# Performance work log

Hardware: AMD Instinct MI355X
Metric: run time of the kernel (lower is better)

## Reference

```python
import jax, jax.numpy as jnp
import numpy as np

NEG_INF = -1e30  # underflows to exactly 0 after softmax in fp32, matching -inf masking


def setup_inputs() -> dict:
    key = jax.random.key(0)
    k1, k2, k3, k4, k5, k6 = jax.random.split(key, 6)
    B, T, D = 4, 4096, 2048
    P, Lmax, c = 1024, 8, 128
    h = jax.random.normal(k1, (B, T, D), dtype=jnp.float32)
    phrase_mask = jax.random.randint(k2, (B, P, Lmax), 0, 2) > 0
    phrase_token_idx = jax.random.randint(k3, (B, P, Lmax), 0, T)
    W_kv = jax.random.normal(k4, (c, D), dtype=jnp.float32) * 0.02
    W_z = jax.random.normal(k5, (c, D), dtype=jnp.float32) * 0.02
    B_pos = jax.random.normal(k6, (Lmax, c), dtype=jnp.float32) * 0.02
    return {"h": h, "phrase_mask": phrase_mask, "phrase_token_idx": phrase_token_idx,
            "W_kv": W_kv, "W_z": W_z, "B_pos": B_pos}


def reference(h, phrase_mask, phrase_token_idx, W_kv, W_z, B_pos):
    B, P, Lmax = phrase_mask.shape
    D = h.shape[-1]
    # Gather phrase tokens: (B, P, Lmax, D)
    idx_flat = phrase_token_idx.reshape(B, P * Lmax)
    h_phrase = jnp.take_along_axis(h, idx_flat[:, :, None], axis=1).reshape(B, P, Lmax, D)
    # Dual thin projections (D -> c)
    c_tok = jnp.einsum('bpld,cd->bplc', h_phrase, W_kv)
    z_tok = jnp.einsum('bpld,cd->bplc', h_phrase, W_z) + B_pos[None, None, :, :]
    # Masked softmax over the phrase-slot dim Lmax
    z_masked = jnp.where(phrase_mask[..., None], z_tok, NEG_INF)
    gates = jax.nn.softmax(z_masked, axis=2)
    any_token = jnp.any(phrase_mask, axis=2)[:, :, None, None]
    gates = jnp.where(any_token, gates, 0.0)
    # Weighted reduce over slots -> (B, P, c)
    return jnp.sum(gates * c_tok, axis=2)
```

## Files before the change

### kernel.cpp

```cpp
#include <hip/hip_runtime.h>
#include <hip/hip_bf16.h>

#define DIM   2048
#define NC    256
#define CDIM  128
#define HALFCZ (16384u * 256u)

typedef __attribute__((ext_vector_type(8))) short short8;
typedef __attribute__((ext_vector_type(4))) float f32x4;

static __device__ __forceinline__ unsigned short f2bf(float f) {
    union { float f; unsigned u; } v; v.f = f;
    return (unsigned short)((v.u + 0x7fffu + ((v.u >> 16) & 1u)) >> 16);
}

static __device__ __forceinline__ short8 cvt8(float4 a, float4 b) {
    union { __hip_bfloat162 h2[4]; short8 s; } u;
    u.h2[0] = __float22bfloat162_rn(float2{a.x, a.y});
    u.h2[1] = __float22bfloat162_rn(float2{a.z, a.w});
    u.h2[2] = __float22bfloat162_rn(float2{b.x, b.y});
    u.h2[3] = __float22bfloat162_rn(float2{b.z, b.w});
    return u.s;
}

static __device__ __forceinline__ float2 ld2bf(const unsigned short* p) {
    unsigned v = *(const unsigned*)p;
    union { unsigned u; float f; } lo, hi;
    lo.u = v << 16;
    hi.u = v & 0xffff0000u;
    return float2{lo.f, hi.f};
}

#define BARRIER() { asm volatile("s_waitcnt lgkmcnt(0)" ::: "memory"); \
                    __builtin_amdgcn_s_barrier(); }

__global__ __launch_bounds__(256) void convert_w(const float* __restrict__ Wkv,
                                                 const float* __restrict__ Wz,
                                                 unsigned short* __restrict__ Wp) {
    int tid = blockIdx.x * 256 + threadIdx.x;
    int l = tid & 63;
    int s = (tid >> 6) & 63;
    int f = tid >> 12;
    int n = f * 16 + (l & 15);
    int k = s * 32 + ((l >> 4) << 3);
    const float* src = (n < CDIM) ? (Wkv + (size_t)n * DIM + k)
                                  : (Wz + (size_t)(n - CDIM) * DIM + k);
    float4 f0 = *(const float4*)src;
    float4 f1 = *(const float4*)(src + 4);
    *(short8*)(Wp + (size_t)tid * 8) = cvt8(f0, f1);
}

__global__ __launch_bounds__(256) void gemm_hw(
    const float* __restrict__ H,
    const unsigned short* __restrict__ Wp,
    unsigned short* __restrict__ CZp)
{
    __shared__ unsigned char As[2 * 64 * 128];

    const int tid    = threadIdx.x;
    const int lane   = tid & 63;
    const int wave   = tid >> 6;
    const int wn     = wave * 64;
    const int bid    = blockIdx.x;
    const int kslice = bid & 1;
    const int m0     = (bid >> 1) * 64;

    unsigned short* CZout = CZp + (size_t)kslice * HALFCZ;

    const int srow  = tid >> 2;
    const int scolf = (tid & 3) * 16;
    const float* gA = H + (size_t)(m0 + srow) * DIM + kslice * 1024 + scolf;
    const int swz   = (srow & 7) << 4;
    const int soff0 = (srow * 128 + scolf * 2) ^ swz;
    const int soff1 = (srow * 128 + scolf * 2 + 16) ^ swz;

    const unsigned short* wpb = Wp + (size_t)(wave * 4) * 32768 + lane * 8;

    f32x4 acc[4][4] = {};
    float4 p0[4], p1[4];
    short8 b0[2][4], b1[2][4];

#define LOADA(P, KT) { \
    _Pragma("unroll") \
    for (int q = 0; q < 4; ++q) P[q] = *(const float4*)(gA + (KT) * 64 + q * 4); }

#define LOADB(B, KT) { \
    _Pragma("unroll") \
    for (int ks = 0; ks < 2; ++ks) \
        _Pragma("unroll") \
        for (int j = 0; j < 4; ++j) \
            B[ks][j] = *(const short8*)(wpb + (size_t)j * 32768 + ((kslice << 5) + (KT) * 2 + ks) * 512); }

#define WRITES(BUFB, P) { \
    short8 lo_ = cvt8(P[0], P[1]); \
    short8 hi_ = cvt8(P[2], P[3]); \
    *(short8*)(As + (BUFB) + soff0) = lo_; \
    *(short8*)(As + (BUFB) + soff1) = hi_; }

#define COMPUTE(BUFB, B) { \
    short8 a_[2][4]; \
    _Pragma("unroll") \
    for (int ks = 0; ks < 2; ++ks) \
        _Pragma("unroll") \
        for (int i = 0; i < 4; ++i) { \
            int row_ = i * 16 + (lane & 15); \
            int off_ = (row_ * 128 + ks * 64 + ((lane >> 4) << 4)) ^ ((row_ & 7) << 4); \
            a_[ks][i] = *(const short8*)(As + (BUFB) + off_); \
        } \
    __builtin_amdgcn_s_setprio(1); \
    _Pragma("unroll") \
    for (int ks = 0; ks < 2; ++ks) \
        _Pragma("unroll") \
        for (int i = 0; i < 4; ++i) \
            _Pragma("unroll") \
            for (int j = 0; j < 4; ++j) \
                acc[i][j] = __builtin_amdgcn_mfma_f32_16x16x32_bf16(a_[ks][i], B[ks][j], acc[i][j], 0, 0, 0); \
    __builtin_amdgcn_s_setprio(0); }

    LOADA(p0, 0);
    LOADB(b0, 0);
    WRITES(0, p0);
    LOADA(p1, 1);
    BARRIER();

    for (int it = 0; it < 16; it += 2) {
        if (it + 2 < 16) LOADA(p0, it + 2);
        LOADB(b1, it + 1);
        WRITES(8192, p1);
        COMPUTE(0, b0);
        BARRIER();

        if (it + 3 < 16) LOADA(p1, it + 3);
        if (it + 2 < 16) { LOADB(b0, it + 2); WRITES(0, p0); }
        COMPUTE(8192, b1);
        BARRIER();
    }

    #pragma unroll
    for (int i = 0; i < 4; ++i)
        #pragma unroll
        for (int j = 0; j < 4; ++j)
            #pragma unroll
            for (int r = 0; r < 4; ++r) {
                int row = m0 + i * 16 + (lane >> 4) * 4 + r;
                int col = wn + j * 16 + (lane & 15);
                CZout[(size_t)row * NC + col] = f2bf(acc[i][j][r]);
            }
#undef LOADA
#undef LOADB
#undef WRITES
#undef COMPUTE
}

__global__ __launch_bounds__(256) void finalize(
    const unsigned short* __restrict__ CZp,
    const int*   __restrict__ mask,
    const int*   __restrict__ idx,
    const float* __restrict__ Bpos,
    float*       __restrict__ out)
{
    const unsigned short* CZ0 = CZp;
    const unsigned short* CZ1 = CZp + HALFCZ;

    int t  = threadIdx.x;
    int lp = t & 63;
    int q  = blockIdx.x * 4 + (t >> 6);
    q = __builtin_amdgcn_readfirstlane(q);
    int b  = q >> 10;
    int ce = lp * 2;

    int rows[8];
    unsigned mbits = 0;
    #pragma unroll
    for (int l = 0; l < 8; ++l) {
        int m   = mask[q * 8 + l];
        int tok = idx[q * 8 + l];
        rows[l] = b * 4096 + tok;
        if (m) mbits |= 1u << l;
    }

    float2 z[8], c[8];
    float2 mx = {-1e30f, -1e30f};
    #pragma unroll
    for (int l = 0; l < 8; ++l) {
        if (mbits & (1u << l)) {
            size_t base = (size_t)rows[l] * NC;
            float2 z0 = ld2bf(CZ0 + base + CDIM + ce);
            float2 z1 = ld2bf(CZ1 + base + CDIM + ce);
            float2 bp = *(const float2*)(Bpos + l * CDIM + ce);
            z[l] = float2{z0.x + z1.x + bp.x, z0.y + z1.y + bp.y};
            float2 c0 = ld2bf(CZ0 + base + ce);
            float2 c1 = ld2bf(CZ1 + base + ce);
            c[l] = float2{c0.x + c1.x, c0.y + c1.y};
            mx.x = fmaxf(mx.x, z[l].x);
            mx.y = fmaxf(mx.y, z[l].y);
        }
    }

    float2 num = {0.f, 0.f}, den = {0.f, 0.f};
    #pragma unroll
    for (int l = 0; l < 8; ++l) {
        if (mbits & (1u << l)) {
            float wx = __expf(z[l].x - mx.x);
            float wy = __expf(z[l].y - mx.y);
            den.x += wx;            den.y += wy;
            num.x += wx * c[l].x;   num.y += wy * c[l].y;
        }
    }
    float2 r = mbits ? float2{num.x / den.x, num.y / den.y} : float2{0.f, 0.f};
    *(float2*)(out + (size_t)q * CDIM + ce) = r;
}

extern "C" void kernel_launch(void* const* d_in, const int* in_sizes, int n_in,
                              void* d_out, int out_size, void* d_ws, size_t ws_size,
                              hipStream_t stream) {
    const float* h    = (const float*)d_in[0];
    const int*   mask = (const int*)d_in[1];
    const int*   idx  = (const int*)d_in[2];
    const float* Wkv  = (const float*)d_in[3];
    const float* Wz   = (const float*)d_in[4];
    const float* Bpos = (const float*)d_in[5];
    float* out = (float*)d_out;

    unsigned short* Wp  = (unsigned short*)d_ws;
    unsigned short* CZp = (unsigned short*)((char*)d_ws + 2 * 1024 * 1024);

    convert_w<<<256, 256, 0, stream>>>(Wkv, Wz, Wp);
    gemm_hw<<<512, 256, 0, stream>>>(h, Wp, CZp);
    finalize<<<1024, 256, 0, stream>>>(CZp, mask, idx, Bpos, out);
}
```

Measured before the change: 44.06 us.

## Split GEMM block across eight waves with narrower per-wave N tiles

The projection GEMM now launches 512 threads per block instead of 256. Each of the eight waves computes a 64x32 output slice instead of 64x64, and each thread stages half as much of H into LDS per k-step. Per-wave accumulator and B-fragment registers are halved, which allows more waves in flight to hide global-load latency. In exchange, every wave still reads the full A tile from LDS, so LDS read traffic per MFMA doubles, and there are more waves taking part in each barrier.

```diff
diff --git a/kernel.cpp b/kernel.cpp
--- a/kernel.cpp
+++ b/kernel.cpp
@@ -50,7 +50,7 @@
     *(short8*)(Wp + (size_t)tid * 8) = cvt8(f0, f1);
 }
 
-__global__ __launch_bounds__(256) void gemm_hw(
+__global__ __launch_bounds__(512, 4) void gemm_hw(
     const float* __restrict__ H,
     const unsigned short* __restrict__ Wp,
     unsigned short* __restrict__ CZp)
@@ -60,42 +60,37 @@
     const int tid    = threadIdx.x;
     const int lane   = tid & 63;
     const int wave   = tid >> 6;
-    const int wn     = wave * 64;
+    const int wn     = wave * 32;
     const int bid    = blockIdx.x;
     const int kslice = bid & 1;
     const int m0     = (bid >> 1) * 64;
 
     unsigned short* CZout = CZp + (size_t)kslice * HALFCZ;
 
-    const int srow  = tid >> 2;
-    const int scolf = (tid & 3) * 16;
-    const float* gA = H + (size_t)(m0 + srow) * DIM + kslice * 1024 + scolf;
-    const int swz   = (srow & 7) << 4;
-    const int soff0 = (srow * 128 + scolf * 2) ^ swz;
-    const int soff1 = (srow * 128 + scolf * 2 + 16) ^ swz;
-
-    const unsigned short* wpb = Wp + (size_t)(wave * 4) * 32768 + lane * 8;
-
-    f32x4 acc[4][4] = {};
-    float4 p0[4], p1[4];
-    short8 b0[2][4], b1[2][4];
-
-#define LOADA(P, KT) { \
-    _Pragma("unroll") \
-    for (int q = 0; q < 4; ++q) P[q] = *(const float4*)(gA + (KT) * 64 + q * 4); }
+    const int srow = tid >> 3;
+    const int scol = (tid & 7) * 8;
+    const float* gA = H + (size_t)(m0 + srow) * DIM + kslice * 1024 + scol;
+    const int soff = (srow * 128 + scol * 2) ^ ((srow & 7) << 4);
+
+    const unsigned short* wpb = Wp + (size_t)(wave * 2) * 32768 + lane * 8;
+
+    f32x4 acc[4][2] = {};
+    float4 pa0, pb0, pa1, pb1;
+    short8 b0[2][2], b1[2][2];
+
+#define LOADA(pa, pb, KT) { \
+    pa = *(const float4*)(gA + (KT) * 64); \
+    pb = *(const float4*)(gA + (KT) * 64 + 4); }
 
 #define LOADB(B, KT) { \
     _Pragma("unroll") \
     for (int ks = 0; ks < 2; ++ks) \
         _Pragma("unroll") \
-        for (int j = 0; j < 4; ++j) \
+        for (int j = 0; j < 2; ++j) \
             B[ks][j] = *(const short8*)(wpb + (size_t)j * 32768 + ((kslice << 5) + (KT) * 2 + ks) * 512); }
 
-#define WRITES(BUFB, P) { \
-    short8 lo_ = cvt8(P[0], P[1]); \
-    short8 hi_ = cvt8(P[2], P[3]); \
-    *(short8*)(As + (BUFB) + soff0) = lo_; \
-    *(short8*)(As + (BUFB) + soff1) = hi_; }
+#define WRITES(BUFB, pa, pb) { \
+    *(short8*)(As + (BUFB) + soff) = cvt8(pa, pb); }
 
 #define COMPUTE(BUFB, B) { \
     short8 a_[2][4]; \
@@ -113,25 +108,25 @@
         _Pragma("unroll") \
         for (int i = 0; i < 4; ++i) \
             _Pragma("unroll") \
-            for (int j = 0; j < 4; ++j) \
+            for (int j = 0; j < 2; ++j) \
                 acc[i][j] = __builtin_amdgcn_mfma_f32_16x16x32_bf16(a_[ks][i], B[ks][j], acc[i][j], 0, 0, 0); \
     __builtin_amdgcn_s_setprio(0); }
 
-    LOADA(p0, 0);
+    LOADA(pa0, pb0, 0);
     LOADB(b0, 0);
-    WRITES(0, p0);
-    LOADA(p1, 1);
+    WRITES(0, pa0, pb0);
+    LOADA(pa1, pb1, 1);
     BARRIER();
 
     for (int it = 0; it < 16; it += 2) {
-        if (it + 2 < 16) LOADA(p0, it + 2);
+        if (it + 2 < 16) LOADA(pa0, pb0, it + 2);
         LOADB(b1, it + 1);
-        WRITES(8192, p1);
+        WRITES(8192, pa1, pb1);
         COMPUTE(0, b0);
         BARRIER();
 
-        if (it + 3 < 16) LOADA(p1, it + 3);
-        if (it + 2 < 16) { LOADB(b0, it + 2); WRITES(0, p0); }
+        if (it + 3 < 16) LOADA(pa1, pb1, it + 3);
+        if (it + 2 < 16) { LOADB(b0, it + 2); WRITES(0, pa0, pb0); }
         COMPUTE(8192, b1);
         BARRIER();
     }
@@ -139,7 +134,7 @@
     #pragma unroll
     for (int i = 0; i < 4; ++i)
         #pragma unroll
-        for (int j = 0; j < 4; ++j)
+        for (int j = 0; j < 2; ++j)
             #pragma unroll
             for (int r = 0; r < 4; ++r) {
                 int row = m0 + i * 16 + (lane >> 4) * 4 + r;
@@ -226,6 +221,6 @@
     unsigned short* CZp = (unsigned short*)((char*)d_ws + 2 * 1024 * 1024);
 
     convert_w<<<256, 256, 0, stream>>>(Wkv, Wz, Wp);
-    gemm_hw<<<512, 256, 0, stream>>>(h, Wp, CZp);
+    gemm_hw<<<512, 512, 0, stream>>>(h, Wp, CZp);
     finalize<<<1024, 256, 0, stream>>>(CZp, mask, idx, Bpos, out);
 }
```

Result: faster. 42.01 us, median of 3 (-4.6%).
